# Kernel optimization log

Measured on AMD Instinct MI355X. Metric: run time of the kernel, lower is better.

## Reference

```python
import jax, jax.numpy as jnp
import numpy as np

N = 50000
E = 1600000
F_IN = 256
DIMS = 64
N_CLS = 16
R = 8


def glorot(key, shape):
    fan = shape[-2] + shape[-1] if len(shape) >= 2 else shape[-1] * 2
    std = jnp.sqrt(6.0 / fan)
    return jax.random.uniform(key, shape, jnp.float32, -std, std)


def setup_inputs() -> dict:
    key = jax.random.key(0)
    ks = jax.random.split(key, 12)
    x = jax.random.normal(ks[0], (N, F_IN), jnp.float32)
    edge_index = jax.random.randint(ks[1], (2, E), 0, N)
    edge_weight = jax.random.uniform(ks[2], (E,), jnp.float32)
    edge_color = jax.random.randint(ks[3], (E,), 0, R)
    W1 = glorot(ks[4], (R, F_IN, DIMS))
    atten1 = glorot(ks[5], (R, 2 * DIMS))
    root1 = glorot(ks[6], (F_IN, DIMS))
    bias1 = jnp.zeros((DIMS,), jnp.float32)
    W2 = glorot(ks[7], (R, DIMS, N_CLS))
    atten2 = glorot(ks[8], (R, 2 * N_CLS))
    root2 = glorot(ks[9], (DIMS, N_CLS))
    bias2 = jnp.zeros((N_CLS,), jnp.float32)
    return dict(x=x, edge_index=edge_index, edge_weight=edge_weight,
                edge_color=edge_color, W1=W1, atten1=atten1, root1=root1,
                bias1=bias1, W2=W2, atten2=atten2, root2=root2, bias2=bias2)


def wrgat_conv(x, src, dst, ew, ec, W, atten, root, bias):
    # x: [N, f_in]; W: [R, f_in, d]; atten: [R, 2d]
    d = W.shape[-1]
    xr = jnp.einsum('nf,rfd->rnd', x, W)            # [R, N, d] per-relation projection
    xi = xr[ec, dst]                                 # [E, d] dst (x_i)
    xj = xr[ec, src]                                 # [E, d] src (x_j)
    a_i = atten[:, :d][ec]                           # [E, d]
    a_j = atten[:, d:][ec]
    s = jnp.sum(a_i * xi + a_j * xj, axis=-1)        # [E]
    s = jax.nn.leaky_relu(s, 0.2)
    # segment softmax over (relation, destination) groups
    seg = ec * N + dst                               # [E], each edge belongs to one relation
    nseg = R * N
    m = jax.ops.segment_max(s, seg, num_segments=nseg)
    m = jnp.where(jnp.isfinite(m), m, 0.0)           # empty segments -> 0
    e = jnp.exp(s - m[seg])
    denom = jax.ops.segment_sum(e, seg, num_segments=nseg)
    alpha = e / jnp.maximum(denom[seg], 1e-16)
    msg = (alpha * ew)[:, None] * xj                 # [E, d]
    summed = jax.ops.segment_sum(msg, seg, num_segments=nseg).reshape(R, N, d)
    cnt = jax.ops.segment_sum(jnp.ones_like(ew), seg, num_segments=nseg).reshape(R, N, 1)
    out = (summed / jnp.maximum(cnt, 1.0)).sum(axis=0)  # mean aggr per relation, summed over relations
    return out + x @ root + bias


def reference(x, edge_index, edge_weight, edge_color, W1, atten1, root1, bias1,
              W2, atten2, root2, bias2):
    src, dst = edge_index[0], edge_index[1]          # PyG flow source_to_target: x_j=src, x_i=dst
    h = wrgat_conv(x, src, dst, edge_weight, edge_color, W1, atten1, root1, bias1)
    h = jax.nn.relu(h)                               # dropout p=0 -> identity
    h = wrgat_conv(h, src, dst, edge_weight, edge_color, W2, atten2, root2, bias2)
    return jax.nn.log_softmax(h, axis=1)
```

## Files before the change

### kernel.cpp

```cpp
#include <hip/hip_runtime.h>
#include <math.h>

#define N_NODES 50000
#define N_EDGES 1600000
#define F_IN    256
#define DIMS    64
#define N_CLS   16
#define R_REL   8
#define CAP     96

#define PROJ_BLKS 3519
#define CSR_BLKS  6250
#define FRONT_BLKS (PROJ_BLKS + CSR_BLKS)

typedef short bf16x8 __attribute__((ext_vector_type(8)));
typedef float f32x4  __attribute__((ext_vector_type(4)));
typedef unsigned int u32;
typedef const __attribute__((address_space(1))) u32* gas_ptr;
typedef __attribute__((address_space(3))) u32* las_ptr;

__device__ __forceinline__ void async16(const void* g, void* l) {
    __builtin_amdgcn_global_load_lds((gas_ptr)g, (las_ptr)l, 16, 0, 0);
}

__device__ __forceinline__ unsigned short f2bf(float f) {
    unsigned u = __float_as_uint(f);
    unsigned r = (u + 0x7fffu + ((u >> 16) & 1u)) >> 16;
    return (unsigned short)r;
}
__device__ __forceinline__ float bf2f(unsigned short u) {
    return __uint_as_float(((unsigned)u) << 16);
}

__global__ __launch_bounds__(256) void cvt_x_kernel(
        const float* __restrict__ x, ushort* __restrict__ xb) {
    int i4 = blockIdx.x * 256 + threadIdx.x;
    float4 v = ((const float4*)x)[i4];
    ushort4 o;
    o.x = f2bf(v.x); o.y = f2bf(v.y); o.z = f2bf(v.z); o.w = f2bf(v.w);
    ((ushort4*)xb)[i4] = o;
}

__global__ __launch_bounds__(256) void cvt_w_kernel(
        const float* __restrict__ W1, const float* __restrict__ root1,
        ushort* __restrict__ wt1) {
    int idx = blockIdx.x * 256 + threadIdx.x;
    int r = idx >> 14, rem = idx & 16383;
    int n = rem >> 8, k = rem & 255;
    float v = (r < 8) ? W1[((size_t)r * F_IN + k) * DIMS + n]
                      : root1[(size_t)k * DIMS + n];
    wt1[idx] = f2bf(v);
}

#define BM 128
__global__ __launch_bounds__(256, 6) void front_kernel(
        const ushort* __restrict__ xb, const ushort* __restrict__ wt1,
        const float* __restrict__ at1,
        ushort* __restrict__ xr1b, float* __restrict__ hroot,
        float* __restrict__ si1, float* __restrict__ sj1,
        const int* __restrict__ ei, const int* __restrict__ ecol,
        const float* __restrict__ ew, int* __restrict__ fill,
        unsigned long long* __restrict__ rec) {
    __shared__ ushort xs[BM * 64];
    const int bid = blockIdx.x;
    const int t = threadIdx.x;

    int pb = -1, cb = -1;
    if (bid < 2 * PROJ_BLKS) { if (bid & 1) cb = bid >> 1; else pb = bid >> 1; }
    else cb = PROJ_BLKS + (bid - 2 * PROJ_BLKS);

    if (cb >= 0) {
        int e = cb * 256 + t;
        int s = ei[e], d = ei[N_EDGES + e], c = ecol[e];
        float w_ = ew[e];
        int p = atomicAdd(&fill[d], 1);
        int idx = (p < CAP) ? d * CAP + p : N_NODES * CAP;
        unsigned long long rv =
            ((unsigned long long)__float_as_uint(w_) << 32)
            | (unsigned)(s | (c << 16));
        __builtin_nontemporal_store(rv, &rec[idx]);
        return;
    }

    const int r = pb / 391;
    const int node0 = (pb % 391) * BM;
    const ushort* wrow = wt1 + (size_t)r * 64 * 256;

    const int w = t >> 6, lane = t & 63;
    const int lane15 = lane & 15, quad = lane >> 4;
    const int row0 = w * 32 + lane15;
    const int sw0 = row0 & 7;

    f32x4 acc[2][4];
    #pragma unroll
    for (int a = 0; a < 2; ++a)
        #pragma unroll
        for (int b = 0; b < 4; ++b)
            acc[a][b] = (f32x4){0.f, 0.f, 0.f, 0.f};

    for (int s = 0; s < 4; ++s) {
        __syncthreads();
        #pragma unroll
        for (int c = 0; c < 4; ++c) {
            int slot = c * 256 + t;
            int row = slot >> 3, k8p = slot & 7;
            int k8 = k8p ^ (row & 7);
            int node = node0 + row;
            if (node >= N_NODES) node = N_NODES - 1;
            async16(&xb[(size_t)node * 256 + s * 64 + k8 * 8],
                    &xs[(c * 256 + w * 64) * 8]);
        }
        __syncthreads();
        #pragma unroll
        for (int kk = 0; kk < 2; ++kk) {
            int k8 = kk * 4 + quad;
            int aidx = row0 * 64 + ((k8 ^ sw0) << 3);
            bf16x8 a0 = *(const bf16x8*)&xs[aidx];
            bf16x8 a1 = *(const bf16x8*)&xs[aidx + 16 * 64];
            int kg = s * 64 + kk * 32 + quad * 8;
            #pragma unroll
            for (int nt = 0; nt < 4; ++nt) {
                bf16x8 b = *(const bf16x8*)&wrow[(size_t)(nt * 16 + lane15) * 256 + kg];
                acc[0][nt] = __builtin_amdgcn_mfma_f32_16x16x32_bf16(a0, b, acc[0][nt], 0, 0, 0);
                acc[1][nt] = __builtin_amdgcn_mfma_f32_16x16x32_bf16(a1, b, acc[1][nt], 0, 0, 0);
            }
        }
    }

    const float* at = at1 + r * 128;
    #pragma unroll
    for (int mt = 0; mt < 2; ++mt) {
        float pi[4] = {0.f, 0.f, 0.f, 0.f};
        float pj[4] = {0.f, 0.f, 0.f, 0.f};
        #pragma unroll
        for (int nt = 0; nt < 4; ++nt) {
            int gcol = nt * 16 + lane15;
            float ai = 0.f, aj = 0.f;
            if (r < 8) { ai = at[gcol]; aj = at[64 + gcol]; }
            #pragma unroll
            for (int reg = 0; reg < 4; ++reg) {
                float v = acc[mt][nt][reg];
                int grow = node0 + w * 32 + mt * 16 + quad * 4 + reg;
                if (grow < N_NODES) {
                    if (r < 8)
                        xr1b[((size_t)r * N_NODES + grow) * 64 + gcol] = f2bf(v);
                    else
                        hroot[(size_t)grow * 64 + gcol] = v;
                }
                pi[reg] += ai * v;
                pj[reg] += aj * v;
            }
        }
        if (r < 8) {
            #pragma unroll
            for (int reg = 0; reg < 4; ++reg) {
                float s_ = pi[reg], u_ = pj[reg];
                #pragma unroll
                for (int off = 1; off < 16; off <<= 1) {
                    s_ += __shfl_xor(s_, off, 64);
                    u_ += __shfl_xor(u_, off, 64);
                }
                if (lane15 == 0) {
                    int grow = node0 + w * 32 + mt * 16 + quad * 4 + reg;
                    if (grow < N_NODES) {
                        si1[r * N_NODES + grow] = s_;
                        sj1[r * N_NODES + grow] = u_;
                    }
                }
            }
        }
    }
}

__global__ __launch_bounds__(256) void agg1s_kernel(
        const unsigned long long* __restrict__ rec, const int* __restrict__ fill,
        const float* __restrict__ si, const float* __restrict__ sj,
        const ushort* __restrict__ xr1b, const float* __restrict__ hroot,
        const float* __restrict__ bias1, float* __restrict__ h) {
    __shared__ int   esrc[4][CAP];
    __shared__ float ecoef[4][CAP];
    __shared__ float sden[4][8];
    __shared__ int   scnt[4][8];
    __shared__ float ssi[4][8];
    const int t = threadIdx.x;
    const int w = t >> 6, lane = t & 63;
    const int d = blockIdx.x * 4 + w;
    if (lane < 8) {
        sden[w][lane] = 0.f; scnt[w][lane] = 0;
        ssi[w][lane] = si[lane * N_NODES + d];
    }
    const int n = min(fill[d], CAP);
    const int base = d * CAP;
    float ex[2] = {0.f, 0.f}, ww[2] = {0.f, 0.f};
    int cc[2] = {0, 0};
    #pragma unroll
    for (int ii = 0; ii < 2; ++ii) {
        int i = lane + ii * 64;
        if (i < n) {
            unsigned long long rv = rec[base + i];
            int px = (int)(unsigned)rv;
            int s = px & 0xffff, c = (px >> 16) & 0x7fff;
            esrc[w][i] = px;
            float sc = ssi[w][c] + sj[c * N_NODES + s];
            sc = sc > 0.f ? sc : 0.2f * sc;
            float e = __expf(sc);
            ex[ii] = e; cc[ii] = c; ww[ii] = __uint_as_float((unsigned)(rv >> 32));
            atomicAdd(&sden[w][c], e);
            atomicAdd(&scnt[w][c], 1);
        }
    }
    #pragma unroll
    for (int ii = 0; ii < 2; ++ii) {
        int i = lane + ii * 64;
        if (i < n)
            ecoef[w][i] = ex[ii] / fmaxf(sden[w][cc[ii]], 1e-16f)
                          * ww[ii] / (float)scnt[w][cc[ii]];
    }
    float a0 = 0.f, a1 = 0.f, a2 = 0.f, a3 = 0.f;
    int i = 0;
    for (; i + 4 <= n; i += 4) {
        int p0 = esrc[w][i], p1 = esrc[w][i + 1];
        int p2 = esrc[w][i + 2], p3 = esrc[w][i + 3];
        float c0 = ecoef[w][i], c1 = ecoef[w][i + 1];
        float c2 = ecoef[w][i + 2], c3 = ecoef[w][i + 3];
        int r0 = (p0 >> 16) * N_NODES + (p0 & 0xffff);
        int r1 = (p1 >> 16) * N_NODES + (p1 & 0xffff);
        int r2 = (p2 >> 16) * N_NODES + (p2 & 0xffff);
        int r3 = (p3 >> 16) * N_NODES + (p3 & 0xffff);
        a0 += c0 * bf2f(xr1b[(size_t)r0 * 64 + lane]);
        a1 += c1 * bf2f(xr1b[(size_t)r1 * 64 + lane]);
        a2 += c2 * bf2f(xr1b[(size_t)r2 * 64 + lane]);
        a3 += c3 * bf2f(xr1b[(size_t)r3 * 64 + lane]);
    }
    for (; i < n; ++i) {
        int p0 = esrc[w][i];
        int r0 = (p0 >> 16) * N_NODES + (p0 & 0xffff);
        a0 += ecoef[w][i] * bf2f(xr1b[(size_t)r0 * 64 + lane]);
    }
    float acc = (a0 + a1) + (a2 + a3) + hroot[(size_t)d * 64 + lane] + bias1[lane];
    h[(size_t)d * 64 + lane] = fmaxf(acc, 0.f);
}

__global__ __launch_bounds__(256) void proj2_kernel(
        const float* __restrict__ h, const float* __restrict__ W2,
        const float* __restrict__ atten2, ushort* __restrict__ xr2b,
        float* __restrict__ si2, float* __restrict__ sj2) {
    __shared__ float w2sh[8][64][16];
    __shared__ float a2sh[8][32];
    __shared__ float hsh[32][65];
    const int t = threadIdx.x;
    for (int i = t; i < R_REL * DIMS * N_CLS; i += 256)
        w2sh[i >> 10][(i >> 4) & 63][i & 15] = W2[i];
    if (t < R_REL * 2 * N_CLS) a2sh[t >> 5][t & 31] = atten2[t];
    const int node0 = blockIdx.x * 32;
    for (int i = t; i < 32 * 64; i += 256) {
        int nn = i >> 6, kk = i & 63;
        int node = node0 + nn;
        hsh[nn][kk] = (node < N_NODES) ? h[(size_t)node * 64 + kk] : 0.f;
    }
    __syncthreads();
    const int nl = t & 31, r = t >> 5;
    const int node = node0 + nl;
    float acc[16] = {};
    #pragma unroll 4
    for (int k = 0; k < 64; ++k) {
        float hv = hsh[nl][k];
        #pragma unroll
        for (int c = 0; c < 16; ++c) acc[c] += hv * w2sh[r][k][c];
    }
    if (node < N_NODES) {
        float si = 0.f, sj = 0.f;
        size_t base = ((size_t)r * N_NODES + node) * 16;
        #pragma unroll
        for (int c = 0; c < 16; ++c) {
            si += a2sh[r][c] * acc[c];
            sj += a2sh[r][16 + c] * acc[c];
        }
        #pragma unroll
        for (int c4 = 0; c4 < 4; ++c4) {
            ushort4 o;
            o.x = f2bf(acc[c4 * 4 + 0]); o.y = f2bf(acc[c4 * 4 + 1]);
            o.z = f2bf(acc[c4 * 4 + 2]); o.w = f2bf(acc[c4 * 4 + 3]);
            *(ushort4*)&xr2b[base + c4 * 4] = o;
        }
        si2[r * N_NODES + node] = si;
        sj2[r * N_NODES + node] = sj;
    }
}

__global__ __launch_bounds__(256) void agg2s_kernel(
        const unsigned long long* __restrict__ rec, const int* __restrict__ fill,
        const float* __restrict__ si, const float* __restrict__ sj,
        const ushort* __restrict__ xr2b, const float* __restrict__ h,
        const float* __restrict__ root2, const float* __restrict__ bias2,
        float* __restrict__ out) {
    __shared__ float rsh[64][17];
    __shared__ float hsh[4][64];
    __shared__ int   esrc[4][CAP];
    __shared__ float ecoef[4][CAP];
    __shared__ float sden[4][8];
    __shared__ int   scnt[4][8];
    __shared__ float ssi[4][8];
    const int t = threadIdx.x;
    for (int i = t; i < DIMS * N_CLS; i += 256) rsh[i >> 4][i & 15] = root2[i];
    const int w = t >> 6, lane = t & 63;
    const int d = blockIdx.x * 4 + w;
    hsh[w][lane] = h[(size_t)d * 64 + lane];
    if (lane < 8) {
        sden[w][lane] = 0.f; scnt[w][lane] = 0;
        ssi[w][lane] = si[lane * N_NODES + d];
    }
    const int n = min(fill[d], CAP);
    const int base = d * CAP;
    float ex[2] = {0.f, 0.f}, ww[2] = {0.f, 0.f};
    int cc[2] = {0, 0};
    #pragma unroll
    for (int ii = 0; ii < 2; ++ii) {
        int i = lane + ii * 64;
        if (i < n) {
            unsigned long long rv = rec[base + i];
            int px = (int)(unsigned)rv;
            int s = px & 0xffff, c = (px >> 16) & 0x7fff;
            esrc[w][i] = px;
            float sc = ssi[w][c] + sj[c * N_NODES + s];
            sc = sc > 0.f ? sc : 0.2f * sc;
            float e = __expf(sc);
            ex[ii] = e; cc[ii] = c; ww[ii] = __uint_as_float((unsigned)(rv >> 32));
            atomicAdd(&sden[w][c], e);
            atomicAdd(&scnt[w][c], 1);
        }
    }
    #pragma unroll
    for (int ii = 0; ii < 2; ++ii) {
        int i = lane + ii * 64;
        if (i < n)
            ecoef[w][i] = ex[ii] / fmaxf(sden[w][cc[ii]], 1e-16f)
                          * ww[ii] / (float)scnt[w][cc[ii]];
    }
    __syncthreads();
    const int sub = lane >> 4, cd = lane & 15;
    float acc = 0.f;
    for (int i = sub; i < n; i += 4) {
        int p = esrc[w][i];
        int row = (p >> 16) * N_NODES + (p & 0xffff);
        acc += ecoef[w][i] * bf2f(xr2b[(size_t)row * 16 + cd]);
    }
    #pragma unroll
    for (int k0 = 0; k0 < 16; ++k0) {
        int k = sub * 16 + k0;
        acc += hsh[w][k] * rsh[k][cd];
    }
    acc += __shfl_xor(acc, 16, 64);
    acc += __shfl_xor(acc, 32, 64);
    if (sub == 0) {
        acc += bias2[cd];
        float m = acc;
        #pragma unroll
        for (int off = 8; off; off >>= 1) m = fmaxf(m, __shfl_xor(m, off, 16));
        float ex2 = expf(acc - m);
        float ssum = ex2;
        #pragma unroll
        for (int off = 8; off; off >>= 1) ssum += __shfl_xor(ssum, off, 16);
        out[(size_t)d * 16 + cd] = acc - m - logf(ssum);
    }
}

extern "C" void kernel_launch(void* const* d_in, const int* in_sizes, int n_in,
                              void* d_out, int out_size, void* d_ws, size_t ws_size,
                              hipStream_t stream) {
    const float* x     = (const float*)d_in[0];
    const int*   ei    = (const int*)  d_in[1];
    const float* ew    = (const float*)d_in[2];
    const int*   ecol  = (const int*)  d_in[3];
    const float* W1    = (const float*)d_in[4];
    const float* at1   = (const float*)d_in[5];
    const float* root1 = (const float*)d_in[6];
    const float* b1    = (const float*)d_in[7];
    const float* W2    = (const float*)d_in[8];
    const float* at2   = (const float*)d_in[9];
    const float* root2 = (const float*)d_in[10];
    const float* b2    = (const float*)d_in[11];
    float* out = (float*)d_out;
    float* ws  = (float*)d_ws;

    ushort*   xb    = (ushort*)(ws + 0);
    ushort*   wt1   = (ushort*)(ws + 6400000);
    ushort*   xr1b  = (ushort*)(ws + 6480000);
    float*    hroot = ws + 19280000;
    ushort*   xr2b  = (ushort*)(ws + 22480000);
    float*    si1   = ws + 25680000;
    float*    sj1   = ws + 26080000;
    float*    si2   = ws + 26480000;
    float*    sj2   = ws + 26880000;
    int*      fill  = (int*)(ws + 27280000);
    float*    h     = ws + 27330000;
    unsigned long long* rec = (unsigned long long*)(ws + 30530000);

    hipMemsetAsync(fill, 0, (size_t)N_NODES * 4, stream);

    cvt_x_kernel<<<12500, 256, 0, stream>>>(x, xb);
    cvt_w_kernel<<<576, 256, 0, stream>>>(W1, root1, wt1);
    front_kernel<<<FRONT_BLKS, 256, 0, stream>>>(xb, wt1, at1, xr1b, hroot,
                                                 si1, sj1, ei, ecol, ew, fill, rec);
    agg1s_kernel<<<12500, 256, 0, stream>>>(rec, fill, si1, sj1, xr1b, hroot, b1, h);
    proj2_kernel<<<1563, 256, 0, stream>>>(h, W2, at2, xr2b, si2, sj2);
    agg2s_kernel<<<12500, 256, 0, stream>>>(rec, fill, si2, sj2, xr2b, h, root2, b2, out);
}
```

Before: 422.4 us.

## Load node tile once and loop over all relations in front kernel

Each projection block now stages a 64-node by full-K tile of x into LDS once and keeps the A fragments in registers. It then loops over all 9 weight matrices (8 relations plus root), so x is no longer re-read once per relation. The CSR-building blocks now handle two edges per thread with vectorized loads, and the block interleaving changes to one projection block per five. The trade-offs are higher LDS and register use, with occupancy reduced to 4 waves, and fewer, longer-running projection blocks.

```diff
diff --git a/kernel.cpp b/kernel.cpp
--- a/kernel.cpp
+++ b/kernel.cpp
@@ -9,8 +9,9 @@
 #define R_REL   8
 #define CAP     96
 
-#define PROJ_BLKS 3519
-#define CSR_BLKS  6250
+#define BM      64
+#define PROJ_BLKS 782
+#define CSR_BLKS  3125
 #define FRONT_BLKS (PROJ_BLKS + CSR_BLKS)
 
 typedef short bf16x8 __attribute__((ext_vector_type(8)));
@@ -52,8 +53,7 @@
     wt1[idx] = f2bf(v);
 }
 
-#define BM 128
-__global__ __launch_bounds__(256, 6) void front_kernel(
+__global__ __launch_bounds__(256, 4) void front_kernel(
         const ushort* __restrict__ xb, const ushort* __restrict__ wt1,
         const float* __restrict__ at1,
         ushort* __restrict__ xr1b, float* __restrict__ hroot,
@@ -61,75 +61,78 @@
         const int* __restrict__ ei, const int* __restrict__ ecol,
         const float* __restrict__ ew, int* __restrict__ fill,
         unsigned long long* __restrict__ rec) {
-    __shared__ ushort xs[BM * 64];
+    __shared__ ushort xs[BM * 256];
     const int bid = blockIdx.x;
     const int t = threadIdx.x;
 
     int pb = -1, cb = -1;
-    if (bid < 2 * PROJ_BLKS) { if (bid & 1) cb = bid >> 1; else pb = bid >> 1; }
-    else cb = PROJ_BLKS + (bid - 2 * PROJ_BLKS);
+    {
+        int q = bid / 5, rm = bid - q * 5;
+        if (rm == 0 && q < PROJ_BLKS) pb = q;
+        else cb = bid - min(q + (rm != 0 ? 1 : 0), PROJ_BLKS);
+    }
 
     if (cb >= 0) {
-        int e = cb * 256 + t;
-        int s = ei[e], d = ei[N_EDGES + e], c = ecol[e];
-        float w_ = ew[e];
-        int p = atomicAdd(&fill[d], 1);
-        int idx = (p < CAP) ? d * CAP + p : N_NODES * CAP;
-        unsigned long long rv =
-            ((unsigned long long)__float_as_uint(w_) << 32)
-            | (unsigned)(s | (c << 16));
-        __builtin_nontemporal_store(rv, &rec[idx]);
+        int idx = cb * 256 + t;
+        int2  s2 = ((const int2*)ei)[idx];
+        int2  d2 = ((const int2*)(ei + N_EDGES))[idx];
+        int2  c2 = ((const int2*)ecol)[idx];
+        float2 w2 = ((const float2*)ew)[idx];
+        int p0 = atomicAdd(&fill[d2.x], 1);
+        int p1 = atomicAdd(&fill[d2.y], 1);
+        unsigned long long r0 =
+            ((unsigned long long)__float_as_uint(w2.x) << 32)
+            | (unsigned)(s2.x | (c2.x << 16));
+        unsigned long long r1 =
+            ((unsigned long long)__float_as_uint(w2.y) << 32)
+            | (unsigned)(s2.y | (c2.y << 16));
+        int i0 = (p0 < CAP) ? d2.x * CAP + p0 : N_NODES * CAP;
+        int i1 = (p1 < CAP) ? d2.y * CAP + p1 : N_NODES * CAP;
+        __builtin_nontemporal_store(r0, &rec[i0]);
+        __builtin_nontemporal_store(r1, &rec[i1]);
         return;
     }
 
-    const int r = pb / 391;
-    const int node0 = (pb % 391) * BM;
-    const ushort* wrow = wt1 + (size_t)r * 64 * 256;
-
+    const int node0 = pb * BM;
     const int w = t >> 6, lane = t & 63;
     const int lane15 = lane & 15, quad = lane >> 4;
-    const int row0 = w * 32 + lane15;
+    const int row0 = w * 16 + lane15;
     const int sw0 = row0 & 7;
 
-    f32x4 acc[2][4];
-    #pragma unroll
-    for (int a = 0; a < 2; ++a)
-        #pragma unroll
-        for (int b = 0; b < 4; ++b)
-            acc[a][b] = (f32x4){0.f, 0.f, 0.f, 0.f};
-
-    for (int s = 0; s < 4; ++s) {
-        __syncthreads();
-        #pragma unroll
-        for (int c = 0; c < 4; ++c) {
-            int slot = c * 256 + t;
-            int row = slot >> 3, k8p = slot & 7;
-            int k8 = k8p ^ (row & 7);
-            int node = node0 + row;
-            if (node >= N_NODES) node = N_NODES - 1;
-            async16(&xb[(size_t)node * 256 + s * 64 + k8 * 8],
-                    &xs[(c * 256 + w * 64) * 8]);
-        }
-        __syncthreads();
-        #pragma unroll
-        for (int kk = 0; kk < 2; ++kk) {
-            int k8 = kk * 4 + quad;
-            int aidx = row0 * 64 + ((k8 ^ sw0) << 3);
-            bf16x8 a0 = *(const bf16x8*)&xs[aidx];
-            bf16x8 a1 = *(const bf16x8*)&xs[aidx + 16 * 64];
-            int kg = s * 64 + kk * 32 + quad * 8;
+    #pragma unroll
+    for (int c = 0; c < 8; ++c) {
+        int slot = c * 256 + t;
+        int row = slot >> 5, chp = slot & 31;
+        int k8 = chp ^ (row & 7);
+        int node = node0 + row;
+        if (node >= N_NODES) node = N_NODES - 1;
+        async16(&xb[(size_t)node * 256 + k8 * 8],
+                &xs[(c * 256 + w * 64) * 8]);
+    }
+    __syncthreads();
+
+    bf16x8 afr[8];
+    #pragma unroll
+    for (int ks = 0; ks < 8; ++ks) {
+        int k8 = ks * 4 + quad;
+        afr[ks] = *(const bf16x8*)&xs[row0 * 256 + ((k8 ^ sw0) << 3)];
+    }
+
+    for (int r = 0; r < 9; ++r) {
+        const ushort* wrow = wt1 + (size_t)r * 64 * 256;
+        f32x4 acc[4];
+        #pragma unroll
+        for (int nt = 0; nt < 4; ++nt) acc[nt] = (f32x4){0.f, 0.f, 0.f, 0.f};
+        #pragma unroll
+        for (int ks = 0; ks < 8; ++ks) {
+            int kg = ks * 32 + quad * 8;
             #pragma unroll
             for (int nt = 0; nt < 4; ++nt) {
                 bf16x8 b = *(const bf16x8*)&wrow[(size_t)(nt * 16 + lane15) * 256 + kg];
-                acc[0][nt] = __builtin_amdgcn_mfma_f32_16x16x32_bf16(a0, b, acc[0][nt], 0, 0, 0);
-                acc[1][nt] = __builtin_amdgcn_mfma_f32_16x16x32_bf16(a1, b, acc[1][nt], 0, 0, 0);
+                acc[nt] = __builtin_amdgcn_mfma_f32_16x16x32_bf16(afr[ks], b, acc[nt], 0, 0, 0);
             }
         }
-    }
-
-    const float* at = at1 + r * 128;
-    #pragma unroll
-    for (int mt = 0; mt < 2; ++mt) {
+        const float* at = at1 + r * 128;
         float pi[4] = {0.f, 0.f, 0.f, 0.f};
         float pj[4] = {0.f, 0.f, 0.f, 0.f};
         #pragma unroll
@@ -139,8 +142,8 @@
             if (r < 8) { ai = at[gcol]; aj = at[64 + gcol]; }
             #pragma unroll
             for (int reg = 0; reg < 4; ++reg) {
-                float v = acc[mt][nt][reg];
-                int grow = node0 + w * 32 + mt * 16 + quad * 4 + reg;
+                float v = acc[nt][reg];
+                int grow = node0 + w * 16 + quad * 4 + reg;
                 if (grow < N_NODES) {
                     if (r < 8)
                         xr1b[((size_t)r * N_NODES + grow) * 64 + gcol] = f2bf(v);
@@ -161,7 +164,7 @@
                     u_ += __shfl_xor(u_, off, 64);
                 }
                 if (lane15 == 0) {
-                    int grow = node0 + w * 32 + mt * 16 + quad * 4 + reg;
+                    int grow = node0 + w * 16 + quad * 4 + reg;
                     if (grow < N_NODES) {
                         si1[r * N_NODES + grow] = s_;
                         sj1[r * N_NODES + grow] = u_;
```

Measured after the change: 488.2 us. 15.6% more time.

## Keep A fragments in registers and loop all relations per node tile

Applied to the files above, without the earlier changes.

The projection blocks now take a 64-node tile, load each wave's A fragments (full K=256) straight from global memory into registers, and loop over all 9 weight matrices (8 relations plus root) with those registers. This drops the LDS staging, the async global-to-LDS copies and the per-stage barriers, and reads each node's x row once instead of once per relation. The cost is fewer, longer projection blocks (782 instead of 3519), higher register pressure from the 8 held fragments, and weight reads still coming from global/L2 inside the relation loop. The block-count formula is changed so the interleaving with the CSR-fill blocks still covers all edges.

```diff
diff --git a/kernel.cpp b/kernel.cpp
--- a/kernel.cpp
+++ b/kernel.cpp
@@ -9,19 +9,13 @@
 #define R_REL   8
 #define CAP     96
 
-#define PROJ_BLKS 3519
+#define BM      64
+#define PROJ_BLKS 782
 #define CSR_BLKS  6250
-#define FRONT_BLKS (PROJ_BLKS + CSR_BLKS)
+#define FRONT_BLKS (2 * PROJ_BLKS + (CSR_BLKS - PROJ_BLKS))
 
 typedef short bf16x8 __attribute__((ext_vector_type(8)));
 typedef float f32x4  __attribute__((ext_vector_type(4)));
-typedef unsigned int u32;
-typedef const __attribute__((address_space(1))) u32* gas_ptr;
-typedef __attribute__((address_space(3))) u32* las_ptr;
-
-__device__ __forceinline__ void async16(const void* g, void* l) {
-    __builtin_amdgcn_global_load_lds((gas_ptr)g, (las_ptr)l, 16, 0, 0);
-}
 
 __device__ __forceinline__ unsigned short f2bf(float f) {
     unsigned u = __float_as_uint(f);
@@ -52,7 +46,6 @@
     wt1[idx] = f2bf(v);
 }
 
-#define BM 128
 __global__ __launch_bounds__(256, 6) void front_kernel(
         const ushort* __restrict__ xb, const ushort* __restrict__ wt1,
         const float* __restrict__ at1,
@@ -61,7 +54,6 @@
         const int* __restrict__ ei, const int* __restrict__ ecol,
         const float* __restrict__ ew, int* __restrict__ fill,
         unsigned long long* __restrict__ rec) {
-    __shared__ ushort xs[BM * 64];
     const int bid = blockIdx.x;
     const int t = threadIdx.x;
 
@@ -82,54 +74,35 @@
         return;
     }
 
-    const int r = pb / 391;
-    const int node0 = (pb % 391) * BM;
-    const ushort* wrow = wt1 + (size_t)r * 64 * 256;
-
+    const int node0 = pb * BM;
     const int w = t >> 6, lane = t & 63;
     const int lane15 = lane & 15, quad = lane >> 4;
-    const int row0 = w * 32 + lane15;
-    const int sw0 = row0 & 7;
-
-    f32x4 acc[2][4];
-    #pragma unroll
-    for (int a = 0; a < 2; ++a)
-        #pragma unroll
-        for (int b = 0; b < 4; ++b)
-            acc[a][b] = (f32x4){0.f, 0.f, 0.f, 0.f};
-
-    for (int s = 0; s < 4; ++s) {
-        __syncthreads();
-        #pragma unroll
-        for (int c = 0; c < 4; ++c) {
-            int slot = c * 256 + t;
-            int row = slot >> 3, k8p = slot & 7;
-            int k8 = k8p ^ (row & 7);
-            int node = node0 + row;
-            if (node >= N_NODES) node = N_NODES - 1;
-            async16(&xb[(size_t)node * 256 + s * 64 + k8 * 8],
-                    &xs[(c * 256 + w * 64) * 8]);
-        }
-        __syncthreads();
-        #pragma unroll
-        for (int kk = 0; kk < 2; ++kk) {
-            int k8 = kk * 4 + quad;
-            int aidx = row0 * 64 + ((k8 ^ sw0) << 3);
-            bf16x8 a0 = *(const bf16x8*)&xs[aidx];
-            bf16x8 a1 = *(const bf16x8*)&xs[aidx + 16 * 64];
-            int kg = s * 64 + kk * 32 + quad * 8;
+    const int row0 = w * 16 + lane15;
+
+    int node = node0 + row0;
+    if (node >= N_NODES) node = N_NODES - 1;
+
+    bf16x8 afr[8];
+    #pragma unroll
+    for (int ks = 0; ks < 8; ++ks)
+        afr[ks] = *(const bf16x8*)&xb[(size_t)node * 256 + ks * 32 + quad * 8];
+
+    #pragma unroll 1
+    for (int r = 0; r < 9; ++r) {
+        const ushort* wrow = wt1 + (size_t)r * 64 * 256;
+        f32x4 acc[4];
+        #pragma unroll
+        for (int nt = 0; nt < 4; ++nt) acc[nt] = (f32x4){0.f, 0.f, 0.f, 0.f};
+        #pragma unroll
+        for (int ks = 0; ks < 8; ++ks) {
+            int kg = ks * 32 + quad * 8;
             #pragma unroll
             for (int nt = 0; nt < 4; ++nt) {
                 bf16x8 b = *(const bf16x8*)&wrow[(size_t)(nt * 16 + lane15) * 256 + kg];
-                acc[0][nt] = __builtin_amdgcn_mfma_f32_16x16x32_bf16(a0, b, acc[0][nt], 0, 0, 0);
-                acc[1][nt] = __builtin_amdgcn_mfma_f32_16x16x32_bf16(a1, b, acc[1][nt], 0, 0, 0);
+                acc[nt] = __builtin_amdgcn_mfma_f32_16x16x32_bf16(afr[ks], b, acc[nt], 0, 0, 0);
             }
         }
-    }
-
-    const float* at = at1 + r * 128;
-    #pragma unroll
-    for (int mt = 0; mt < 2; ++mt) {
+        const float* at = at1 + r * 128;
         float pi[4] = {0.f, 0.f, 0.f, 0.f};
         float pj[4] = {0.f, 0.f, 0.f, 0.f};
         #pragma unroll
@@ -139,8 +112,8 @@
             if (r < 8) { ai = at[gcol]; aj = at[64 + gcol]; }
             #pragma unroll
             for (int reg = 0; reg < 4; ++reg) {
-                float v = acc[mt][nt][reg];
-                int grow = node0 + w * 32 + mt * 16 + quad * 4 + reg;
+                float v = acc[nt][reg];
+                int grow = node0 + w * 16 + quad * 4 + reg;
                 if (grow < N_NODES) {
                     if (r < 8)
                         xr1b[((size_t)r * N_NODES + grow) * 64 + gcol] = f2bf(v);
@@ -161,7 +134,7 @@
                     u_ += __shfl_xor(u_, off, 64);
                 }
                 if (lane15 == 0) {
-                    int grow = node0 + w * 32 + mt * 16 + quad * 4 + reg;
+                    int grow = node0 + w * 16 + quad * 4 + reg;
                     if (grow < N_NODES) {
                         si1[r * N_NODES + grow] = s_;
                         sj1[r * N_NODES + grow] = u_;
```

Result: slower. 575.0 us (+36.1%).
